# Performance work log

Measured on AMD Instinct MI355X. Metric: run time of the kernel, lower is better.

## Reference

```python
import jax, jax.numpy as jnp
import numpy as np

N_NODES = 100000
N_EDGES = 1600000
IN_C, HID_C, OUT_C = 256, 128, 64


def setup_inputs() -> dict:
    key = jax.random.key(0)
    k_x, k_e, k_w1, k_w2 = jax.random.split(key, 4)
    x = jax.random.normal(k_x, (N_NODES, IN_C), dtype=jnp.float32)
    edge_index = jax.random.randint(k_e, (2, N_EDGES), 0, N_NODES, dtype=jnp.int64)
    # Glorot-ish init scaled like PyG defaults
    W1 = jax.random.normal(k_w1, (IN_C, HID_C), dtype=jnp.float32) * (1.0 / np.sqrt(IN_C))
    b1 = jnp.zeros((HID_C,), dtype=jnp.float32)
    W2 = jax.random.normal(k_w2, (HID_C, OUT_C), dtype=jnp.float32) * (1.0 / np.sqrt(HID_C))
    b2 = jnp.zeros((OUT_C,), dtype=jnp.float32)
    return {"x": x, "edge_index": edge_index, "W1": W1, "b1": b1, "W2": W2, "b2": b2}


def _gcn_norm(edge_index, n_nodes, dtype):
    # PyG gcn_norm: add self-loops, deg over targets, norm = d_i^-1/2 * d_j^-1/2
    loop = jnp.arange(n_nodes, dtype=edge_index.dtype)
    src = jnp.concatenate([edge_index[0], loop])
    dst = jnp.concatenate([edge_index[1], loop])
    deg = jax.ops.segment_sum(jnp.ones_like(dst, dtype=dtype), dst, num_segments=n_nodes)
    dis = jnp.where(deg > 0, jax.lax.rsqrt(jnp.maximum(deg, 1e-12)), 0.0).astype(dtype)
    norm = dis[src] * dis[dst]  # [E + N]
    return src, dst, norm


def _gcn_conv(x, src, dst, norm, W, b, n_nodes):
    h = x @ W                                    # [N, C_out] dense transform first
    msg = h[src] * norm[:, None]                 # edge-wise gather + scale
    agg = jax.ops.segment_sum(msg, dst, num_segments=n_nodes)  # scatter-add
    return agg + b


def reference(x, edge_index, W1, b1, W2, b2):
    n = x.shape[0]
    src, dst, norm = _gcn_norm(edge_index, n, x.dtype)
    h = _gcn_conv(x, src, dst, norm, W1, b1, n)
    out = _gcn_conv(h, src, dst, norm, W2, b2, n)
    return out
```

## Files before the change

### kernel.cpp

```cpp
#include <hip/hip_runtime.h>
#include <math.h>

#define IN_C  256
#define HID_C 128
#define OUT_C 64

typedef short bf16x8 __attribute__((ext_vector_type(8)));
typedef float f32x4  __attribute__((ext_vector_type(4)));

__device__ __forceinline__ unsigned short f2bf(float f) {
    unsigned u = __float_as_uint(f);
    unsigned rounding = 0x7FFFu + ((u >> 16) & 1u);
    return (unsigned short)((u + rounding) >> 16);
}

__global__ void detect_kernel(const void* edges, int E, int n_nodes, int* flag) {
    if (threadIdx.x == 0 && blockIdx.x == 0) {
        const long long* p = (const long long*)edges;
        int k = E < 64 ? E : 64;
        int is64 = 1;
        for (int i = 0; i < k; ++i) {
            long long v = p[i];
            if (v < 0 || v >= n_nodes) { is64 = 0; break; }
        }
        *flag = is64;
    }
}

__device__ __forceinline__ int load_edge(const void* edges, size_t idx, int is64) {
    return is64 ? (int)((const long long*)edges)[idx] : ((const int*)edges)[idx];
}

__global__ void convert_wt(const float* __restrict__ W, unsigned short* __restrict__ Wt,
                           int K, int N) {
    int idx = blockIdx.x * 256 + threadIdx.x;
    if (idx >= K * N) return;
    int k = idx / N, n_ = idx % N;
    Wt[(size_t)n_ * K + k] = f2bf(W[idx]);
}

__global__ void zero8(int* counts8, int n8) {
    int i = blockIdx.x * 256 + threadIdx.x;
    if (i < n8) counts8[i] = 0;
}

__global__ __launch_bounds__(256) void conv_count(
    const float* __restrict__ x, unsigned short* __restrict__ xb, int nconv,
    const void* edges, const int* __restrict__ flag,
    int* counts8, int* __restrict__ rank, int E, int n, int CONV) {
    const int bid = blockIdx.x;
    if (bid < CONV) {
        int t = bid * 256 + threadIdx.x;
        int stride = CONV * 256;
        for (int i = t; i < nconv; i += stride) {
            const float4* p = (const float4*)(x + (size_t)i * 8);
            float4 a = p[0], b = p[1];
            union { unsigned short u[8]; uint4 v; } t8;
            t8.u[0] = f2bf(a.x); t8.u[1] = f2bf(a.y); t8.u[2] = f2bf(a.z); t8.u[3] = f2bf(a.w);
            t8.u[4] = f2bf(b.x); t8.u[5] = f2bf(b.y); t8.u[6] = f2bf(b.z); t8.u[7] = f2bf(b.w);
            *(uint4*)(xb + (size_t)i * 8) = t8.v;
        }
        return;
    }
    int e = (bid - CONV) * 256 + threadIdx.x;
    if (e >= E) return;
    const int f = *flag;
    int d = load_edge(edges, (size_t)E + e, f);
    unsigned xcc = (unsigned)__builtin_amdgcn_s_getreg((3 << 11) | 20) & 7u;
    int rl = atomicAdd(&counts8[(size_t)xcc * n + d], 1);
    rank[e] = rl | (int)(xcc << 28);
}

__global__ void scan8_block_dis(const int* __restrict__ counts8, int* __restrict__ xoff,
                                int* __restrict__ deg, int* __restrict__ excl,
                                int* __restrict__ blockSums, float* __restrict__ dis, int n) {
    __shared__ int tmp[256];
    int i = blockIdx.x * 256 + threadIdx.x;
    int v = 0;
    if (i < n) {
        int s = 0;
        #pragma unroll
        for (int xg = 0; xg < 8; ++xg) {
            int c = counts8[(size_t)xg * n + i];
            xoff[(size_t)xg * n + i] = s;
            s += c;
        }
        v = s;
        deg[i] = s;
        dis[i] = rsqrtf((float)s + 1.0f);
    }
    tmp[threadIdx.x] = v;
    __syncthreads();
    for (int off = 1; off < 256; off <<= 1) {
        int t = (threadIdx.x >= off) ? tmp[threadIdx.x - off] : 0;
        __syncthreads();
        if (threadIdx.x >= off) tmp[threadIdx.x] += t;
        __syncthreads();
    }
    if (i < n) excl[i] = tmp[threadIdx.x] - v;
    if (threadIdx.x == 255) blockSums[blockIdx.x] = tmp[255];
}

__global__ void scan_sums(int* blockSums, int nb) {
    __shared__ int tmp[512];
    int v = (threadIdx.x < nb) ? blockSums[threadIdx.x] : 0;
    tmp[threadIdx.x] = v;
    __syncthreads();
    for (int off = 1; off < 512; off <<= 1) {
        int t = (threadIdx.x >= off) ? tmp[threadIdx.x - off] : 0;
        __syncthreads();
        if (threadIdx.x >= off) tmp[threadIdx.x] += t;
        __syncthreads();
    }
    if (threadIdx.x < nb) blockSums[threadIdx.x] = tmp[threadIdx.x] - v;
}

__global__ void add_offsets(int* __restrict__ excl, const int* __restrict__ blockSums, int n) {
    int i = blockIdx.x * 256 + threadIdx.x;
    if (i < n) excl[i] += blockSums[blockIdx.x];
}

__global__ __launch_bounds__(256) void fill_csr_rank(
    const void* edges, const int* __restrict__ flag,
    const int* __restrict__ row_ptr, const int* __restrict__ xoff,
    const int* __restrict__ rank, int* __restrict__ ssrc, int E, int n) {
    const int f = *flag;
    int e = blockIdx.x * 256 + threadIdx.x;
    if (e >= E) return;
    int d = load_edge(edges, (size_t)E + e, f);
    int s = load_edge(edges, e, f);
    int rk = rank[e];
    int pos = row_ptr[d] + xoff[(size_t)(rk >> 28) * n + d] + (rk & 0x0FFFFFFF);
    ssrc[pos] = s;
}

template<int TN, int K>
__global__ __launch_bounds__(256) void gemm_mfma_bb(
    const unsigned short* __restrict__ A, const unsigned short* __restrict__ Wt,
    const float* __restrict__ dis, unsigned short* __restrict__ C, int M) {
    constexpr int TM = 64, KC = 64, NCF = TN / 16;
    __shared__ __align__(16) unsigned short A_lds[TM * KC];
    __shared__ __align__(16) unsigned short B_lds[TN * KC];
    const int tid  = threadIdx.x;
    const int wave = tid >> 6;
    const int lane = tid & 63;
    const int q    = lane >> 4;
    const int cl   = lane & 15;
    const long long row0 = (long long)blockIdx.x * TM;

    f32x4 acc[NCF];
    const f32x4 fzero = {0.f, 0.f, 0.f, 0.f};
    #pragma unroll
    for (int cf = 0; cf < NCF; ++cf) acc[cf] = fzero;

    for (int k0 = 0; k0 < K; k0 += KC) {
        #pragma unroll
        for (int p = 0; p < 2; ++p) {
            int i = p * 256 + tid;
            int r = i >> 3, c = i & 7;
            uint4 v = *(const uint4*)(A + (row0 + r) * K + k0 + c * 8);
            *(uint4*)((char*)A_lds + r * 128 + ((c ^ (r & 7)) * 16)) = v;
        }
        #pragma unroll
        for (int p = 0; p < TN / 32; ++p) {
            int i = p * 256 + tid;
            int bc = i >> 3, c = i & 7;
            uint4 v = *(const uint4*)(Wt + (size_t)bc * K + k0 + c * 8);
            *(uint4*)((char*)B_lds + bc * 128 + ((c ^ (bc & 7)) * 16)) = v;
        }
        __syncthreads();
        #pragma unroll
        for (int ksub = 0; ksub < 2; ++ksub) {
            const int cidx = ksub * 4 + q;
            const int r = wave * 16 + cl;
            bf16x8 af = *(const bf16x8*)((const char*)A_lds + r * 128 + ((cidx ^ (r & 7)) * 16));
            #pragma unroll
            for (int cf = 0; cf < NCF; ++cf) {
                const int bc = cf * 16 + cl;
                bf16x8 bfr = *(const bf16x8*)((const char*)B_lds + bc * 128 + ((cidx ^ (bc & 7)) * 16));
                acc[cf] = __builtin_amdgcn_mfma_f32_16x16x32_bf16(af, bfr, acc[cf], 0, 0, 0);
            }
        }
        __syncthreads();
    }
    #pragma unroll
    for (int j = 0; j < 4; ++j) {
        long long row = row0 + wave * 16 + q * 4 + j;
        if (row >= M) continue;
        float d = dis[row];
        #pragma unroll
        for (int cf = 0; cf < NCF; ++cf)
            C[row * TN + cf * 16 + cl] = f2bf(acc[cf][j] * d);
    }
}

template<int C, int NPB, bool OBF>
__global__ __launch_bounds__(256) void gather_layer_bf(
    const unsigned short* __restrict__ hs, const int* __restrict__ row_ptr,
    const int* __restrict__ deg, const int* __restrict__ ssrc,
    const float* __restrict__ dis, const float* __restrict__ bias,
    void* __restrict__ outp, int n) {
    constexpr int TPN = C / 8;
    const int local = threadIdx.x / TPN;
    const int lane  = threadIdx.x % TPN;
    const int i = blockIdx.x * NPB + local;
    if (i >= n) return;
    const uint4* h4 = (const uint4*)hs;
    float di = dis[i];
    float acc[8] = {};
    auto accum = [&](uint4 u) {
        acc[0] += __uint_as_float(u.x << 16);
        acc[1] += __uint_as_float(u.x & 0xffff0000u);
        acc[2] += __uint_as_float(u.y << 16);
        acc[3] += __uint_as_float(u.y & 0xffff0000u);
        acc[4] += __uint_as_float(u.z << 16);
        acc[5] += __uint_as_float(u.z & 0xffff0000u);
        acc[6] += __uint_as_float(u.w << 16);
        acc[7] += __uint_as_float(u.w & 0xffff0000u);
    };
    accum(h4[(size_t)i * TPN + lane]);
    const int start = row_ptr[i];
    const int cnt   = deg[i];
    const int* sp = ssrc + start;
    int j = 0;
    for (; j + 4 <= cnt; j += 4) {
        int s0 = sp[j], s1 = sp[j + 1], s2 = sp[j + 2], s3 = sp[j + 3];
        uint4 v0 = h4[(size_t)s0 * TPN + lane];
        uint4 v1 = h4[(size_t)s1 * TPN + lane];
        uint4 v2 = h4[(size_t)s2 * TPN + lane];
        uint4 v3 = h4[(size_t)s3 * TPN + lane];
        accum(v0); accum(v1); accum(v2); accum(v3);
    }
    for (; j < cnt; ++j) accum(h4[(size_t)sp[j] * TPN + lane]);
    const float* bp = bias + lane * 8;
    float o[8];
    #pragma unroll
    for (int k = 0; k < 8; ++k) o[k] = bp[k] + di * acc[k];
    if constexpr (OBF) {
        union { unsigned short u[8]; uint4 v; } t8;
        #pragma unroll
        for (int k = 0; k < 8; ++k) t8.u[k] = f2bf(o[k]);
        *(uint4*)((unsigned short*)outp + (size_t)i * C + lane * 8) = t8.v;
    } else {
        float* op = (float*)outp + (size_t)i * C + lane * 8;
        *(float4*)op = make_float4(o[0], o[1], o[2], o[3]);
        *(float4*)(op + 4) = make_float4(o[4], o[5], o[6], o[7]);
    }
}

extern "C" void kernel_launch(void* const* d_in, const int* in_sizes, int n_in,
                              void* d_out, int out_size, void* d_ws, size_t ws_size,
                              hipStream_t stream) {
    const float* x     = (const float*)d_in[0];
    const void*  edges = d_in[1];
    const float* W1    = (const float*)d_in[2];
    const float* b1    = (const float*)d_in[3];
    const float* W2    = (const float*)d_in[4];
    const float* b2    = (const float*)d_in[5];
    float* out = (float*)d_out;

    const int n = in_sizes[0] / IN_C;
    const int E = in_sizes[1] / 2;
    const int nb = (n + 255) / 256;

    char* ws = (char*)d_ws;
    size_t off = 0;
    auto alloc = [&](size_t bytes) { char* p = ws + off; off += (bytes + 255) & ~(size_t)255; return p; };
    int*   flag      = (int*)  alloc(4);
    int*   counts8   = (int*)  alloc((size_t)n * 8 * 4);
    int*   xoff      = (int*)  alloc((size_t)n * 8 * 4);
    int*   deg       = (int*)  alloc((size_t)n * 4);
    int*   row_ptr   = (int*)  alloc((size_t)n * 4);
    int*   blockSums = (int*)  alloc(512 * 4);
    float* dis       = (float*)alloc((size_t)n * 4);
    int*   rank      = (int*)  alloc((size_t)E * 4);
    int*   ssrc      = (int*)  alloc((size_t)E * 4);
    unsigned short* xb   = (unsigned short*)alloc((size_t)(n + 64) * IN_C * 2);
    unsigned short* hs   = (unsigned short*)alloc((size_t)(n + 64) * HID_C * 2);
    unsigned short* aggb = (unsigned short*)alloc((size_t)(n + 64) * HID_C * 2);

    detect_kernel<<<1, 64, 0, stream>>>(edges, E, n, flag);
    convert_wt<<<(IN_C * HID_C + 255) / 256, 256, 0, stream>>>(W1, (unsigned short*)hs, IN_C, HID_C);
    unsigned short* Wt1 = (unsigned short*)alloc((size_t)IN_C * HID_C * 2);
    unsigned short* Wt2 = (unsigned short*)alloc((size_t)HID_C * OUT_C * 2);
    convert_wt<<<(IN_C * HID_C + 255) / 256, 256, 0, stream>>>(W1, Wt1, IN_C, HID_C);
    convert_wt<<<(HID_C * OUT_C + 255) / 256, 256, 0, stream>>>(W2, Wt2, HID_C, OUT_C);
    zero8<<<(n * 8 + 255) / 256, 256, 0, stream>>>(counts8, n * 8);

    const int CONV = 512;
    const int nconv = n * IN_C / 8;
    conv_count<<<CONV + (E + 255) / 256, 256, 0, stream>>>(
        x, xb, nconv, edges, flag, counts8, rank, E, n, CONV);

    scan8_block_dis<<<nb, 256, 0, stream>>>(counts8, xoff, deg, row_ptr, blockSums, dis, n);
    scan_sums<<<1, 512, 0, stream>>>(blockSums, nb);
    add_offsets<<<nb, 256, 0, stream>>>(row_ptr, blockSums, n);

    fill_csr_rank<<<(E + 255) / 256, 256, 0, stream>>>(edges, flag, row_ptr, xoff, rank, ssrc, E, n);

    gemm_mfma_bb<HID_C, IN_C><<<(n + 63) / 64, 256, 0, stream>>>(xb, Wt1, dis, hs, n);
    gather_layer_bf<HID_C, 16, true><<<(n + 15) / 16, 256, 0, stream>>>(hs, row_ptr, deg, ssrc, dis, b1, aggb, n);

    gemm_mfma_bb<OUT_C, HID_C><<<(n + 63) / 64, 256, 0, stream>>>(aggb, Wt2, dis, hs, n);
    gather_layer_bf<OUT_C, 32, false><<<(n + 31) / 32, 256, 0, stream>>>(hs, row_ptr, deg, ssrc, dis, b2, out, n);
}
```

Before: 248.1 us.

## Fuse CSR fill into first GEMM launch and batch edges per thread

```diff
diff --git a/kernel.cpp b/kernel.cpp
--- a/kernel.cpp
+++ b/kernel.cpp
@@ -62,13 +62,23 @@
         }
         return;
     }
-    int e = (bid - CONV) * 256 + threadIdx.x;
-    if (e >= E) return;
     const int f = *flag;
-    int d = load_edge(edges, (size_t)E + e, f);
+    const int e0 = (bid - CONV) * 1024 + threadIdx.x;
     unsigned xcc = (unsigned)__builtin_amdgcn_s_getreg((3 << 11) | 20) & 7u;
-    int rl = atomicAdd(&counts8[(size_t)xcc * n + d], 1);
-    rank[e] = rl | (int)(xcc << 28);
+    int d[4]; bool v[4];
+    #pragma unroll
+    for (int k = 0; k < 4; ++k) {
+        int e = e0 + k * 256;
+        v[k] = (e < E);
+        d[k] = v[k] ? load_edge(edges, (size_t)E + e, f) : 0;
+    }
+    int rl[4];
+    #pragma unroll
+    for (int k = 0; k < 4; ++k)
+        if (v[k]) rl[k] = atomicAdd(&counts8[(size_t)xcc * n + d[k]], 1);
+    #pragma unroll
+    for (int k = 0; k < 4; ++k)
+        if (v[k]) rank[e0 + k * 256] = rl[k] | (int)(xcc << 28);
 }
 
 __global__ void scan8_block_dis(const int* __restrict__ counts8, int* __restrict__ xoff,
@@ -120,18 +130,97 @@
     if (i < n) excl[i] += blockSums[blockIdx.x];
 }
 
-__global__ __launch_bounds__(256) void fill_csr_rank(
+template<int TN, int K>
+__global__ __launch_bounds__(256) void fused_gemm_fill(
+    const unsigned short* __restrict__ A, const unsigned short* __restrict__ Wt,
+    const float* __restrict__ dis, unsigned short* __restrict__ C, int M, int G,
     const void* edges, const int* __restrict__ flag,
     const int* __restrict__ row_ptr, const int* __restrict__ xoff,
     const int* __restrict__ rank, int* __restrict__ ssrc, int E, int n) {
-    const int f = *flag;
-    int e = blockIdx.x * 256 + threadIdx.x;
-    if (e >= E) return;
-    int d = load_edge(edges, (size_t)E + e, f);
-    int s = load_edge(edges, e, f);
-    int rk = rank[e];
-    int pos = row_ptr[d] + xoff[(size_t)(rk >> 28) * n + d] + (rk & 0x0FFFFFFF);
-    ssrc[pos] = s;
+    constexpr int TM = 64, KC = 64, NCF = TN / 16;
+    __shared__ __align__(16) unsigned short A_lds[TM * KC];
+    __shared__ __align__(16) unsigned short B_lds[TN * KC];
+    const int bid = blockIdx.x;
+    const bool is_gemm = (bid < 2 * G) && ((bid & 1) == 0);
+
+    if (!is_gemm) {
+        const int fb = (bid < 2 * G) ? (bid >> 1) : (bid - G);
+        const int f = *flag;
+        const int e0 = fb * 1024 + threadIdx.x;
+        int d[4], s[4], rk[4]; bool v[4];
+        #pragma unroll
+        for (int k = 0; k < 4; ++k) {
+            int e = e0 + k * 256;
+            v[k] = (e < E);
+            if (v[k]) {
+                d[k]  = load_edge(edges, (size_t)E + e, f);
+                s[k]  = load_edge(edges, e, f);
+                rk[k] = rank[e];
+            }
+        }
+        #pragma unroll
+        for (int k = 0; k < 4; ++k) {
+            if (v[k]) {
+                int pos = row_ptr[d[k]] + xoff[(size_t)(rk[k] >> 28) * n + d[k]]
+                        + (rk[k] & 0x0FFFFFFF);
+                ssrc[pos] = s[k];
+            }
+        }
+        return;
+    }
+
+    const int g = bid >> 1;
+    const int tid  = threadIdx.x;
+    const int wave = tid >> 6;
+    const int lane = tid & 63;
+    const int q    = lane >> 4;
+    const int cl   = lane & 15;
+    const long long row0 = (long long)g * TM;
+
+    f32x4 acc[NCF];
+    const f32x4 fzero = {0.f, 0.f, 0.f, 0.f};
+    #pragma unroll
+    for (int cf = 0; cf < NCF; ++cf) acc[cf] = fzero;
+
+    for (int k0 = 0; k0 < K; k0 += KC) {
+        #pragma unroll
+        for (int p = 0; p < 2; ++p) {
+            int i = p * 256 + tid;
+            int r = i >> 3, c = i & 7;
+            uint4 v = *(const uint4*)(A + (row0 + r) * K + k0 + c * 8);
+            *(uint4*)((char*)A_lds + r * 128 + ((c ^ (r & 7)) * 16)) = v;
+        }
+        #pragma unroll
+        for (int p = 0; p < TN / 32; ++p) {
+            int i = p * 256 + tid;
+            int bc = i >> 3, c = i & 7;
+            uint4 v = *(const uint4*)(Wt + (size_t)bc * K + k0 + c * 8);
+            *(uint4*)((char*)B_lds + bc * 128 + ((c ^ (bc & 7)) * 16)) = v;
+        }
+        __syncthreads();
+        #pragma unroll
+        for (int ksub = 0; ksub < 2; ++ksub) {
+            const int cidx = ksub * 4 + q;
+            const int r = wave * 16 + cl;
+            bf16x8 af = *(const bf16x8*)((const char*)A_lds + r * 128 + ((cidx ^ (r & 7)) * 16));
+            #pragma unroll
+            for (int cf = 0; cf < NCF; ++cf) {
+                const int bc = cf * 16 + cl;
+                bf16x8 bfr = *(const bf16x8*)((const char*)B_lds + bc * 128 + ((cidx ^ (bc & 7)) * 16));
+                acc[cf] = __builtin_amdgcn_mfma_f32_16x16x32_bf16(af, bfr, acc[cf], 0, 0, 0);
+            }
+        }
+        __syncthreads();
+    }
+    #pragma unroll
+    for (int j = 0; j < 4; ++j) {
+        long long row = row0 + wave * 16 + q * 4 + j;
+        if (row >= M) continue;
+        float d = dis[row];
+        #pragma unroll
+        for (int cf = 0; cf < NCF; ++cf)
+            C[row * TN + cf * 16 + cl] = f2bf(acc[cf][j] * d);
+    }
 }
 
 template<int TN, int K>
@@ -223,13 +312,19 @@
     const int cnt   = deg[i];
     const int* sp = ssrc + start;
     int j = 0;
+    for (; j + 8 <= cnt; j += 8) {
+        uint4 v[8];
+        #pragma unroll
+        for (int k = 0; k < 8; ++k) v[k] = h4[(size_t)sp[j + k] * TPN + lane];
+        #pragma unroll
+        for (int k = 0; k < 8; ++k) accum(v[k]);
+    }
     for (; j + 4 <= cnt; j += 4) {
-        int s0 = sp[j], s1 = sp[j + 1], s2 = sp[j + 2], s3 = sp[j + 3];
-        uint4 v0 = h4[(size_t)s0 * TPN + lane];
-        uint4 v1 = h4[(size_t)s1 * TPN + lane];
-        uint4 v2 = h4[(size_t)s2 * TPN + lane];
-        uint4 v3 = h4[(size_t)s3 * TPN + lane];
-        accum(v0); accum(v1); accum(v2); accum(v3);
+        uint4 v[4];
+        #pragma unroll
+        for (int k = 0; k < 4; ++k) v[k] = h4[(size_t)sp[j + k] * TPN + lane];
+        #pragma unroll
+        for (int k = 0; k < 4; ++k) accum(v[k]);
     }
     for (; j < cnt; ++j) accum(h4[(size_t)sp[j] * TPN + lane]);
     const float* bp = bias + lane * 8;
@@ -278,27 +373,28 @@
     unsigned short* xb   = (unsigned short*)alloc((size_t)(n + 64) * IN_C * 2);
     unsigned short* hs   = (unsigned short*)alloc((size_t)(n + 64) * HID_C * 2);
     unsigned short* aggb = (unsigned short*)alloc((size_t)(n + 64) * HID_C * 2);
+    unsigned short* Wt1  = (unsigned short*)alloc((size_t)IN_C * HID_C * 2);
+    unsigned short* Wt2  = (unsigned short*)alloc((size_t)HID_C * OUT_C * 2);
 
     detect_kernel<<<1, 64, 0, stream>>>(edges, E, n, flag);
-    convert_wt<<<(IN_C * HID_C + 255) / 256, 256, 0, stream>>>(W1, (unsigned short*)hs, IN_C, HID_C);
-    unsigned short* Wt1 = (unsigned short*)alloc((size_t)IN_C * HID_C * 2);
-    unsigned short* Wt2 = (unsigned short*)alloc((size_t)HID_C * OUT_C * 2);
     convert_wt<<<(IN_C * HID_C + 255) / 256, 256, 0, stream>>>(W1, Wt1, IN_C, HID_C);
     convert_wt<<<(HID_C * OUT_C + 255) / 256, 256, 0, stream>>>(W2, Wt2, HID_C, OUT_C);
     zero8<<<(n * 8 + 255) / 256, 256, 0, stream>>>(counts8, n * 8);
 
     const int CONV = 512;
     const int nconv = n * IN_C / 8;
-    conv_count<<<CONV + (E + 255) / 256, 256, 0, stream>>>(
+    conv_count<<<CONV + (E + 1023) / 1024, 256, 0, stream>>>(
         x, xb, nconv, edges, flag, counts8, rank, E, n, CONV);
 
     scan8_block_dis<<<nb, 256, 0, stream>>>(counts8, xoff, deg, row_ptr, blockSums, dis, n);
     scan_sums<<<1, 512, 0, stream>>>(blockSums, nb);
     add_offsets<<<nb, 256, 0, stream>>>(row_ptr, blockSums, n);
 
-    fill_csr_rank<<<(E + 255) / 256, 256, 0, stream>>>(edges, flag, row_ptr, xoff, rank, ssrc, E, n);
-
-    gemm_mfma_bb<HID_C, IN_C><<<(n + 63) / 64, 256, 0, stream>>>(xb, Wt1, dis, hs, n);
+    const int G = (n + 63) / 64;
+    const int F = (E + 1023) / 1024;
+    fused_gemm_fill<HID_C, IN_C><<<G + F, 256, 0, stream>>>(
+        xb, Wt1, dis, hs, n, G, edges, flag, row_ptr, xoff, rank, ssrc, E, n);
+
     gather_layer_bf<HID_C, 16, true><<<(n + 15) / 16, 256, 0, stream>>>(hs, row_ptr, deg, ssrc, dis, b1, aggb, n);
 
     gemm_mfma_bb<OUT_C, HID_C><<<(n + 63) / 64, 256, 0, stream>>>(aggb, Wt2, dis, hs, n);
```

Result: slower. 264.3 us (+6.6%).

## Build CSR via two-level bucket partition with LDS histograms instead of global atomics

Applied to the files above, without the earlier changes.

```diff
diff --git a/kernel.cpp b/kernel.cpp
--- a/kernel.cpp
+++ b/kernel.cpp
@@ -4,6 +4,8 @@
 #define IN_C  256
 #define HID_C 128
 #define OUT_C 64
+#define CHUNK 4096
+#define MAXNB 400
 
 typedef short bf16x8 __attribute__((ext_vector_type(8)));
 typedef float f32x4  __attribute__((ext_vector_type(4)));
@@ -39,19 +41,15 @@
     Wt[(size_t)n_ * K + k] = f2bf(W[idx]);
 }
 
-__global__ void zero8(int* counts8, int n8) {
-    int i = blockIdx.x * 256 + threadIdx.x;
-    if (i < n8) counts8[i] = 0;
-}
-
-__global__ __launch_bounds__(256) void conv_count(
+__global__ __launch_bounds__(1024) void conv_hist(
     const float* __restrict__ x, unsigned short* __restrict__ xb, int nconv,
     const void* edges, const int* __restrict__ flag,
-    int* counts8, int* __restrict__ rank, int E, int n, int CONV) {
+    int* __restrict__ hist, int E, int NB, int CH, int CONV) {
+    __shared__ int h[MAXNB];
     const int bid = blockIdx.x;
     if (bid < CONV) {
-        int t = bid * 256 + threadIdx.x;
-        int stride = CONV * 256;
+        int t = bid * 1024 + threadIdx.x;
+        int stride = CONV * 1024;
         for (int i = t; i < nconv; i += stride) {
             const float4* p = (const float4*)(x + (size_t)i * 8);
             float4 a = p[0], b = p[1];
@@ -62,76 +60,119 @@
         }
         return;
     }
-    int e = (bid - CONV) * 256 + threadIdx.x;
-    if (e >= E) return;
+    const int c = bid - CONV;
+    for (int b = threadIdx.x; b < NB; b += 1024) h[b] = 0;
+    __syncthreads();
     const int f = *flag;
-    int d = load_edge(edges, (size_t)E + e, f);
-    unsigned xcc = (unsigned)__builtin_amdgcn_s_getreg((3 << 11) | 20) & 7u;
-    int rl = atomicAdd(&counts8[(size_t)xcc * n + d], 1);
-    rank[e] = rl | (int)(xcc << 28);
-}
-
-__global__ void scan8_block_dis(const int* __restrict__ counts8, int* __restrict__ xoff,
-                                int* __restrict__ deg, int* __restrict__ excl,
-                                int* __restrict__ blockSums, float* __restrict__ dis, int n) {
+    const int e0 = c * CHUNK + threadIdx.x;
+    #pragma unroll
+    for (int k = 0; k < CHUNK / 1024; ++k) {
+        int e = e0 + k * 1024;
+        if (e < E) {
+            int d = load_edge(edges, (size_t)E + e, f);
+            atomicAdd(&h[d >> 8], 1);
+        }
+    }
+    __syncthreads();
+    for (int b = threadIdx.x; b < NB; b += 1024)
+        hist[(size_t)b * CH + c] = h[b];
+}
+
+__global__ __launch_bounds__(512) void scan_chunks(
+    int* __restrict__ hist, int* __restrict__ bucketTotal, int NB, int CH) {
+    __shared__ int tmp[512];
+    const int b = blockIdx.x;
+    const int t = threadIdx.x;
+    int v = (t < CH) ? hist[(size_t)b * CH + t] : 0;
+    tmp[t] = v;
+    __syncthreads();
+    for (int off = 1; off < 512; off <<= 1) {
+        int u = (t >= off) ? tmp[t - off] : 0;
+        __syncthreads();
+        if (t >= off) tmp[t] += u;
+        __syncthreads();
+    }
+    if (t < CH) hist[(size_t)b * CH + t] = tmp[t] - v;
+    if (t == 511) bucketTotal[b] = tmp[511];
+}
+
+__global__ __launch_bounds__(512) void scan_buckets(int* __restrict__ base, int NB, int Etot) {
+    __shared__ int tmp[512];
+    const int t = threadIdx.x;
+    int v = (t < NB) ? base[t] : 0;
+    tmp[t] = v;
+    __syncthreads();
+    for (int off = 1; off < 512; off <<= 1) {
+        int u = (t >= off) ? tmp[t - off] : 0;
+        __syncthreads();
+        if (t >= off) tmp[t] += u;
+        __syncthreads();
+    }
+    if (t < NB) base[t] = tmp[t] - v;
+    if (t == 0) base[NB] = Etot;
+}
+
+__global__ __launch_bounds__(1024) void partition_edges(
+    const void* edges, const int* __restrict__ flag,
+    const int* __restrict__ chunkBase, const int* __restrict__ bucketBase,
+    unsigned* __restrict__ epart, int E, int NB, int CH) {
+    __shared__ int cur[MAXNB];
+    const int c = blockIdx.x;
+    for (int b = threadIdx.x; b < NB; b += 1024)
+        cur[b] = chunkBase[(size_t)b * CH + c] + bucketBase[b];
+    __syncthreads();
+    const int f = *flag;
+    const int e0 = c * CHUNK + threadIdx.x;
+    #pragma unroll
+    for (int k = 0; k < CHUNK / 1024; ++k) {
+        int e = e0 + k * 1024;
+        if (e < E) {
+            int d = load_edge(edges, (size_t)E + e, f);
+            int s = load_edge(edges, e, f);
+            int pos = atomicAdd(&cur[d >> 8], 1);
+            epart[pos] = (unsigned)s | ((unsigned)(d & 255) << 24);
+        }
+    }
+}
+
+__global__ __launch_bounds__(256) void bucket_sort(
+    const unsigned* __restrict__ epart, const int* __restrict__ bucketBase,
+    int* __restrict__ ssrc, int* __restrict__ deg, int* __restrict__ row_ptr,
+    float* __restrict__ dis, int n) {
+    __shared__ int cnt[256];
     __shared__ int tmp[256];
-    int i = blockIdx.x * 256 + threadIdx.x;
-    int v = 0;
-    if (i < n) {
-        int s = 0;
-        #pragma unroll
-        for (int xg = 0; xg < 8; ++xg) {
-            int c = counts8[(size_t)xg * n + i];
-            xoff[(size_t)xg * n + i] = s;
-            s += c;
-        }
-        v = s;
-        deg[i] = s;
-        dis[i] = rsqrtf((float)s + 1.0f);
-    }
-    tmp[threadIdx.x] = v;
+    __shared__ int cursor[256];
+    const int b = blockIdx.x;
+    const int t = threadIdx.x;
+    const int bstart = bucketBase[b], bend = bucketBase[b + 1];
+    cnt[t] = 0;
+    __syncthreads();
+    for (int i = bstart + t; i < bend; i += 256)
+        atomicAdd(&cnt[epart[i] >> 24], 1);
+    __syncthreads();
+    int v = cnt[t];
+    tmp[t] = v;
     __syncthreads();
     for (int off = 1; off < 256; off <<= 1) {
-        int t = (threadIdx.x >= off) ? tmp[threadIdx.x - off] : 0;
-        __syncthreads();
-        if (threadIdx.x >= off) tmp[threadIdx.x] += t;
-        __syncthreads();
-    }
-    if (i < n) excl[i] = tmp[threadIdx.x] - v;
-    if (threadIdx.x == 255) blockSums[blockIdx.x] = tmp[255];
-}
-
-__global__ void scan_sums(int* blockSums, int nb) {
-    __shared__ int tmp[512];
-    int v = (threadIdx.x < nb) ? blockSums[threadIdx.x] : 0;
-    tmp[threadIdx.x] = v;
-    __syncthreads();
-    for (int off = 1; off < 512; off <<= 1) {
-        int t = (threadIdx.x >= off) ? tmp[threadIdx.x - off] : 0;
-        __syncthreads();
-        if (threadIdx.x >= off) tmp[threadIdx.x] += t;
-        __syncthreads();
-    }
-    if (threadIdx.x < nb) blockSums[threadIdx.x] = tmp[threadIdx.x] - v;
-}
-
-__global__ void add_offsets(int* __restrict__ excl, const int* __restrict__ blockSums, int n) {
-    int i = blockIdx.x * 256 + threadIdx.x;
-    if (i < n) excl[i] += blockSums[blockIdx.x];
-}
-
-__global__ __launch_bounds__(256) void fill_csr_rank(
-    const void* edges, const int* __restrict__ flag,
-    const int* __restrict__ row_ptr, const int* __restrict__ xoff,
-    const int* __restrict__ rank, int* __restrict__ ssrc, int E, int n) {
-    const int f = *flag;
-    int e = blockIdx.x * 256 + threadIdx.x;
-    if (e >= E) return;
-    int d = load_edge(edges, (size_t)E + e, f);
-    int s = load_edge(edges, e, f);
-    int rk = rank[e];
-    int pos = row_ptr[d] + xoff[(size_t)(rk >> 28) * n + d] + (rk & 0x0FFFFFFF);
-    ssrc[pos] = s;
+        int u = (t >= off) ? tmp[t - off] : 0;
+        __syncthreads();
+        if (t >= off) tmp[t] += u;
+        __syncthreads();
+    }
+    int excl = tmp[t] - v;
+    cursor[t] = excl;
+    int node = b * 256 + t;
+    if (node < n) {
+        deg[node] = v;
+        row_ptr[node] = bstart + excl;
+        dis[node] = rsqrtf((float)v + 1.0f);
+    }
+    __syncthreads();
+    for (int i = bstart + t; i < bend; i += 256) {
+        unsigned p = epart[i];
+        int pos = bstart + atomicAdd(&cursor[p >> 24], 1);
+        ssrc[pos] = (int)(p & 0xFFFFFFu);
+    }
 }
 
 template<int TN, int K>
@@ -223,13 +264,19 @@
     const int cnt   = deg[i];
     const int* sp = ssrc + start;
     int j = 0;
+    for (; j + 8 <= cnt; j += 8) {
+        uint4 v[8];
+        #pragma unroll
+        for (int k = 0; k < 8; ++k) v[k] = h4[(size_t)sp[j + k] * TPN + lane];
+        #pragma unroll
+        for (int k = 0; k < 8; ++k) accum(v[k]);
+    }
     for (; j + 4 <= cnt; j += 4) {
-        int s0 = sp[j], s1 = sp[j + 1], s2 = sp[j + 2], s3 = sp[j + 3];
-        uint4 v0 = h4[(size_t)s0 * TPN + lane];
-        uint4 v1 = h4[(size_t)s1 * TPN + lane];
-        uint4 v2 = h4[(size_t)s2 * TPN + lane];
-        uint4 v3 = h4[(size_t)s3 * TPN + lane];
-        accum(v0); accum(v1); accum(v2); accum(v3);
+        uint4 v[4];
+        #pragma unroll
+        for (int k = 0; k < 4; ++k) v[k] = h4[(size_t)sp[j + k] * TPN + lane];
+        #pragma unroll
+        for (int k = 0; k < 4; ++k) accum(v[k]);
     }
     for (; j < cnt; ++j) accum(h4[(size_t)sp[j] * TPN + lane]);
     const float* bp = bias + lane * 8;
@@ -259,44 +306,41 @@
     const float* b2    = (const float*)d_in[5];
     float* out = (float*)d_out;
 
-    const int n = in_sizes[0] / IN_C;
-    const int E = in_sizes[1] / 2;
-    const int nb = (n + 255) / 256;
+    const int n  = in_sizes[0] / IN_C;
+    const int E  = in_sizes[1] / 2;
+    const int NB = (n + 255) / 256;
+    const int CH = (E + CHUNK - 1) / CHUNK;
 
     char* ws = (char*)d_ws;
     size_t off = 0;
     auto alloc = [&](size_t bytes) { char* p = ws + off; off += (bytes + 255) & ~(size_t)255; return p; };
-    int*   flag      = (int*)  alloc(4);
-    int*   counts8   = (int*)  alloc((size_t)n * 8 * 4);
-    int*   xoff      = (int*)  alloc((size_t)n * 8 * 4);
-    int*   deg       = (int*)  alloc((size_t)n * 4);
-    int*   row_ptr   = (int*)  alloc((size_t)n * 4);
-    int*   blockSums = (int*)  alloc(512 * 4);
-    float* dis       = (float*)alloc((size_t)n * 4);
-    int*   rank      = (int*)  alloc((size_t)E * 4);
-    int*   ssrc      = (int*)  alloc((size_t)E * 4);
+    int*   flag       = (int*)  alloc(4);
+    int*   hist       = (int*)  alloc((size_t)NB * CH * 4);
+    int*   bucketBase = (int*)  alloc((size_t)(NB + 1) * 4);
+    int*   deg        = (int*)  alloc((size_t)n * 4);
+    int*   row_ptr    = (int*)  alloc((size_t)n * 4);
+    float* dis        = (float*)alloc((size_t)n * 4);
+    unsigned* epart   = (unsigned*)alloc((size_t)E * 4);
+    int*   ssrc       = (int*)  alloc((size_t)E * 4);
     unsigned short* xb   = (unsigned short*)alloc((size_t)(n + 64) * IN_C * 2);
     unsigned short* hs   = (unsigned short*)alloc((size_t)(n + 64) * HID_C * 2);
     unsigned short* aggb = (unsigned short*)alloc((size_t)(n + 64) * HID_C * 2);
+    unsigned short* Wt1  = (unsigned short*)alloc((size_t)IN_C * HID_C * 2);
+    unsigned short* Wt2  = (unsigned short*)alloc((size_t)HID_C * OUT_C * 2);
 
     detect_kernel<<<1, 64, 0, stream>>>(edges, E, n, flag);
-    convert_wt<<<(IN_C * HID_C + 255) / 256, 256, 0, stream>>>(W1, (unsigned short*)hs, IN_C, HID_C);
-    unsigned short* Wt1 = (unsigned short*)alloc((size_t)IN_C * HID_C * 2);
-    unsigned short* Wt2 = (unsigned short*)alloc((size_t)HID_C * OUT_C * 2);
     convert_wt<<<(IN_C * HID_C + 255) / 256, 256, 0, stream>>>(W1, Wt1, IN_C, HID_C);
     convert_wt<<<(HID_C * OUT_C + 255) / 256, 256, 0, stream>>>(W2, Wt2, HID_C, OUT_C);
-    zero8<<<(n * 8 + 255) / 256, 256, 0, stream>>>(counts8, n * 8);
-
-    const int CONV = 512;
+
+    const int CONV = 256;
     const int nconv = n * IN_C / 8;
-    conv_count<<<CONV + (E + 255) / 256, 256, 0, stream>>>(
-        x, xb, nconv, edges, flag, counts8, rank, E, n, CONV);
-
-    scan8_block_dis<<<nb, 256, 0, stream>>>(counts8, xoff, deg, row_ptr, blockSums, dis, n);
-    scan_sums<<<1, 512, 0, stream>>>(blockSums, nb);
-    add_offsets<<<nb, 256, 0, stream>>>(row_ptr, blockSums, n);
-
-    fill_csr_rank<<<(E + 255) / 256, 256, 0, stream>>>(edges, flag, row_ptr, xoff, rank, ssrc, E, n);
+    conv_hist<<<CONV + CH, 1024, 0, stream>>>(x, xb, nconv, edges, flag, hist, E, NB, CH, CONV);
+
+    scan_chunks<<<NB, 512, 0, stream>>>(hist, bucketBase, NB, CH);
+    scan_buckets<<<1, 512, 0, stream>>>(bucketBase, NB, E);
+
+    partition_edges<<<CH, 1024, 0, stream>>>(edges, flag, hist, bucketBase, epart, E, NB, CH);
+    bucket_sort<<<NB, 256, 0, stream>>>(epart, bucketBase, ssrc, deg, row_ptr, dis, n);
 
     gemm_mfma_bb<HID_C, IN_C><<<(n + 63) / 64, 256, 0, stream>>>(xb, Wt1, dis, hs, n);
     gather_layer_bf<HID_C, 16, true><<<(n + 15) / 16, 256, 0, stream>>>(hs, row_ptr, deg, ssrc, dis, b1, aggb, n);
```

Measured after the change: 200.9 us (median of 2 runs). -19.0%, faster.
